# Optimization experiments

Measured on AMD Instinct MI355X. Metric: run time of the kernel, lower is better.

The kernel has to match this reference:

```python
import jax, jax.numpy as jnp
import numpy as np

B, C, H, W, MODES, RANK = 16, 128, 128, 128, 16, 8


def setup_inputs() -> dict:
    key = jax.random.key(0)
    ks = jax.random.split(key, 8)
    scale = 1.0 / (C * C)
    lr_scale = 0.02
    return {
        "x": jax.random.normal(ks[0], (B, C, H, W), dtype=jnp.float32),
        "w_real": scale * jax.random.normal(ks[1], (C, C, MODES, MODES), dtype=jnp.float32),
        "w_imag": scale * jax.random.normal(ks[2], (C, C, MODES, MODES), dtype=jnp.float32),
        "u_real": lr_scale * jax.random.normal(ks[3], (C, RANK, MODES, MODES), dtype=jnp.float32),
        "u_imag": lr_scale * jax.random.normal(ks[4], (C, RANK, MODES, MODES), dtype=jnp.float32),
        "v_real": lr_scale * jax.random.normal(ks[5], (C, RANK, MODES, MODES), dtype=jnp.float32),
        "v_imag": lr_scale * jax.random.normal(ks[6], (C, RANK, MODES, MODES), dtype=jnp.float32),
        "skip_w": (1.0 / np.sqrt(C)) * jax.random.normal(ks[7], (C, C), dtype=jnp.float32),
    }


def physical_act(x):
    # f(x) = x * exp(-|x|^2)
    return x * jnp.exp(-jnp.abs(x) ** 2)


def reference(x, w_real, w_imag, u_real, u_imag, v_real, v_imag, skip_w):
    Bb, Cc, Hh, Ww = x.shape
    # 1x1 conv skip path == channel matmul
    x_skip = jnp.einsum('oc,bchw->bohw', skip_w, x)
    # FFT to spectral domain: (B, C, H, W//2+1) complex64
    x_ft = jnp.fft.rfft2(x, norm='ortho')
    W_ft = x_ft.shape[-1]
    m1 = min(w_real.shape[-2], Hh)
    m2 = min(w_real.shape[-1], W_ft)
    # truncated-mode complex diagonal operator D (per-frequency channel mix)
    D = (w_real + 1j * w_imag)[:, :, :m1, :m2]          # (O, I, m1, m2)
    x_top = x_ft[:, :, :m1, :m2]                         # (B, I, m1, m2)
    out_top = jnp.einsum('bimn,oimn->bomn', x_top, D)
    # low-rank cross-frequency mixer UV*
    U = (u_real + 1j * u_imag)[:, :, :m1, :m2]           # (O, R, m1, m2)
    V = (v_real + 1j * v_imag)[:, :, :m1, :m2]           # (I, R, m1, m2)
    z = jnp.einsum('bimn,irmn->br', x_top, jnp.conj(V))  # (B, R)
    out_top = out_top + jnp.einsum('ormn,br->bomn', U, z)
    # scatter back into zero-padded full spectrum
    out_ft = jnp.zeros(x_ft.shape, dtype=x_ft.dtype).at[:, :, :m1, :m2].set(out_top)
    x_spectral = jnp.fft.irfft2(out_ft, s=(Hh, Ww), norm='ortho')
    out = x_spectral + x_skip
    return physical_act(out)
```

## Files before the change

kernel.cpp:

```cpp
#include <hip/hip_runtime.h>
#include <math.h>

#define TAB_OFF 0
#define XTOP_OFF 16384
#define Z_OFF (16384 + 1048576)
#define OTOP_OFF (Z_OFF + 256)
#define TF_OFF (OTOP_OFF + 1048576)
#define T2F_OFF (TF_OFF + 4096)
#define SWF_OFF XTOP_OFF

using bf16x8 = __attribute__((ext_vector_type(8))) short;
using s16x4  = __attribute__((ext_vector_type(4))) short;
using f32x16 = __attribute__((ext_vector_type(16))) float;

__device__ inline unsigned short bf_rnd(float v) {
  return (unsigned short)((__float_as_uint(v) + 0x8000u) >> 16);
}
__device__ inline void bf_split(float v, unsigned short& hi, unsigned short& lo) {
  unsigned u = __float_as_uint(v);
  hi = (unsigned short)(u >> 16);
  float r = v - __uint_as_float(u & 0xFFFF0000u);
  lo = (unsigned short)(__float_as_uint(r) >> 16);
}
__device__ inline bf16x8 ldfrag(const unsigned short* p) {
  s16x4 a = *(const s16x4*)p;
  s16x4 b = *(const s16x4*)(p + 4);
  bf16x8 r;
  r[0] = a[0]; r[1] = a[1]; r[2] = a[2]; r[3] = a[3];
  r[4] = b[0]; r[5] = b[1]; r[6] = b[2]; r[7] = b[3];
  return r;
}
__device__ inline bf16x8 ldfrag_sw(const unsigned short* base, int row, int koff) {
  int byte = row * 256 + ((koff * 2) ^ ((row & 7) << 4));
  return ldfrag((const unsigned short*)((const char*)base + byte));
}

__global__ __launch_bounds__(256) void k_tab(float* __restrict__ tab) {
  int idx = blockIdx.x * 256 + threadIdx.x;
  if (idx >= 16384) return;
  int which = idx >> 11, rem = idx & 2047;
  int a, j;
  if (which == 4 || which == 5) { a = rem & 127; j = rem >> 7; }
  else { a = rem >> 4; j = rem & 15; }
  int p = (a * j) & 127;
  float ang = (float)p * (float)(3.14159265358979323846 / 64.0);
  float cv = cosf(ang), sv = sinf(ang);
  float v;
  switch (which) {
    case 0: v = cv * (1.f / 128.f); break;
    case 1: v = -sv * (1.f / 128.f); break;
    case 2: v = cv; break;
    case 3: v = sv; break;
    case 4: v = cv; break;
    case 5: v = sv; break;
    case 6: v = ((rem & 15) == 0 ? 1.f : 2.f) * cv * (1.f / 128.f); break;
    default: v = ((rem & 15) == 0 ? 1.f : 2.f) * (-sv) * (1.f / 128.f); break;
  }
  tab[idx] = v;
}

__global__ __launch_bounds__(256) void k_fprep(unsigned short* __restrict__ tf) {
  int idx = blockIdx.x * 256 + threadIdx.x;
  if (idx >= 4096) return;
  int np = idx >> 7, k = idx & 127;
  int n = np & 15;
  int p = (k * n) & 127;
  float ang = (float)p * (float)(3.14159265358979323846 / 64.0);
  float v = (np < 16 ? cosf(ang) : -sinf(ang)) * (1.f / 128.f);
  unsigned short hi, lo;
  bf_split(v, hi, lo);
  tf[np * 128 + k] = hi;
  tf[4096 + np * 128 + k] = lo;
}

__global__ __launch_bounds__(256) void k_t2prep(const float* __restrict__ tab,
                                                unsigned short* __restrict__ t2f) {
  int idx = blockIdx.x * 256 + threadIdx.x;
  if (idx >= 4096) return;
  int w = idx >> 5, np = idx & 31;
  float v = (np < 16) ? tab[12288 + w * 16 + np] : tab[14336 + w * 16 + (np - 16)];
  t2f[idx] = bf_rnd(v);
}

__global__ __launch_bounds__(256) void k_wprep(const float* __restrict__ sw,
                                               unsigned short* __restrict__ swf) {
  int idx = blockIdx.x * 256 + threadIdx.x;
  if (idx >= 16384) return;
  int o = idx >> 7, k = idx & 127;
  unsigned short hb, lb;
  bf_split(sw[o * 128 + k], hb, lb);
  int kc = k >> 5, ks = (k >> 4) & 1, kh = (k >> 3) & 1, j = k & 7;
  int f0 = (kc * 2 + ks) * 2;
  swf[(f0 + 0) * 2048 + o * 16 + kh * 8 + j] = hb;
  swf[(f0 + 1) * 2048 + o * 16 + kh * 8 + j] = lb;
}

__global__ __launch_bounds__(256) void k_fwd(const float* __restrict__ x,
                                             const unsigned short* __restrict__ tf,
                                             const float* __restrict__ tab,
                                             float* __restrict__ xtop) {
  __shared__ unsigned short Xh[128 * 128];
  __shared__ unsigned short Tfh[32 * 128];
  __shared__ unsigned short Tfl[32 * 128];
  const int c = blockIdx.x, b = blockIdx.y;
  const int t = threadIdx.x;
  const int lane = t & 63, wv = t >> 6;

  #pragma unroll
  for (int it = 0; it < 32; ++it) {
    int idx = it * 256 + t;
    int part = idx >> 12, rem = idx & 4095;
    int row = rem >> 7, k = rem & 127;
    unsigned short v = tf[part * 4096 + rem];
    unsigned short* dst = part ? Tfl : Tfh;
    *(unsigned short*)((char*)dst + row * 256 + ((k * 2) ^ ((row & 7) << 4))) = v;
  }
  const float* img = x + (((size_t)(b * 128 + c)) << 14);
  #pragma unroll
  for (int it = 0; it < 16; ++it) {
    int flat = it * 256 + t;
    int h = flat >> 5, wq = flat & 31;
    float4 v = *(const float4*)(img + (size_t)flat * 4);
    s16x4 pk;
    pk[0] = (short)bf_rnd(v.x); pk[1] = (short)bf_rnd(v.y);
    pk[2] = (short)bf_rnd(v.z); pk[3] = (short)bf_rnd(v.w);
    *(s16x4*)((char*)Xh + h * 256 + ((wq * 8) ^ ((h & 7) << 4))) = pk;
  }
  __syncthreads();

  f32x16 acc;
  #pragma unroll
  for (int e = 0; e < 16; ++e) acc[e] = 0.f;
  const int orow = wv * 32 + (lane & 31);
  const int bcol = lane & 31;
  const int kh8 = (lane >> 5) * 8;
  #pragma unroll
  for (int kc8 = 0; kc8 < 8; ++kc8) {
    int kfull = kc8 * 16 + kh8;
    bf16x8 a  = ldfrag_sw(Xh, orow, kfull);
    bf16x8 th = ldfrag_sw(Tfh, bcol, kfull);
    bf16x8 tl = ldfrag_sw(Tfl, bcol, kfull);
    acc = __builtin_amdgcn_mfma_f32_32x32x16_bf16(a, th, acc, 0, 0, 0);
    acc = __builtin_amdgcn_mfma_f32_32x32x16_bf16(a, tl, acc, 0, 0, 0);
  }
  __syncthreads();

  float* Arp = (float*)Xh;
  float* Aip = Arp + 16 * 132;
  {
    const int col = lane & 31;
    #pragma unroll
    for (int r = 0; r < 16; ++r) {
      int h = wv * 32 + (r & 3) + 8 * (r >> 2) + 4 * (lane >> 5);
      if (col < 16) Arp[col * 132 + h] = acc[r];
      else          Aip[(col - 16) * 132 + h] = acc[r];
    }
  }
  __syncthreads();

  {
    const int m = t >> 4, n = t & 15;
    const float* tc = tab + 8192 + m * 128;
    const float* ts = tab + 10240 + m * 128;
    const float* ar = Arp + n * 132;
    const float* ai = Aip + n * 132;
    float xr = 0.f, xi = 0.f;
    #pragma unroll 8
    for (int h4 = 0; h4 < 128; h4 += 4) {
      float4 av = *(const float4*)(ar + h4);
      float4 iv = *(const float4*)(ai + h4);
      float4 cv = *(const float4*)(tc + h4);
      float4 sv = *(const float4*)(ts + h4);
      xr += av.x * cv.x + iv.x * sv.x;  xi += iv.x * cv.x - av.x * sv.x;
      xr += av.y * cv.y + iv.y * sv.y;  xi += iv.y * cv.y - av.y * sv.y;
      xr += av.z * cv.z + iv.z * sv.z;  xi += iv.z * cv.z - av.z * sv.z;
      xr += av.w * cv.w + iv.w * sv.w;  xi += iv.w * cv.w - av.w * sv.w;
    }
    size_t base = ((size_t)(b * 128 + c)) * 512 + (size_t)(m * 16 + n) * 2;
    xtop[base] = xr; xtop[base + 1] = xi;
  }
}

__global__ __launch_bounds__(256) void k_z(const float* __restrict__ xtop,
                                           const float* __restrict__ vre,
                                           const float* __restrict__ vim,
                                           float* __restrict__ zout) {
  int b = blockIdx.x, ic = blockIdx.y, t = threadIdx.x;
  float zr[8], zi[8];
  #pragma unroll
  for (int r = 0; r < 8; ++r) { zr[r] = 0.f; zi[r] = 0.f; }
  const float* xb = xtop + ((size_t)b * 128) * 512;
  for (int i = ic * 16; i < ic * 16 + 16; ++i) {
    float xr = xb[i * 512 + t * 2], xi = xb[i * 512 + t * 2 + 1];
    #pragma unroll
    for (int r = 0; r < 8; ++r) {
      float vr = vre[(size_t)(i * 8 + r) * 256 + t];
      float vi = vim[(size_t)(i * 8 + r) * 256 + t];
      zr[r] += xr * vr + xi * vi;
      zi[r] += xi * vr - xr * vi;
    }
  }
  #pragma unroll
  for (int r = 0; r < 8; ++r)
    for (int off = 32; off > 0; off >>= 1) {
      zr[r] += __shfl_down(zr[r], off);
      zi[r] += __shfl_down(zi[r], off);
    }
  __shared__ float red[4][16];
  int wid = t >> 6, lane = t & 63;
  if (lane == 0) {
    #pragma unroll
    for (int r = 0; r < 8; ++r) { red[wid][r * 2] = zr[r]; red[wid][r * 2 + 1] = zi[r]; }
  }
  __syncthreads();
  if (t < 16) atomicAdd(&zout[b * 16 + t], red[0][t] + red[1][t] + red[2][t] + red[3][t]);
}

__global__ __launch_bounds__(256) void k_mix(const float* __restrict__ xtop,
                                             const float* __restrict__ wre,
                                             const float* __restrict__ wim,
                                             const float* __restrict__ ure,
                                             const float* __restrict__ uim,
                                             const float* __restrict__ z,
                                             float* __restrict__ otop) {
  int o0 = blockIdx.x * 4, b0 = blockIdx.y * 2, ic = blockIdx.z, t = threadIdx.x;
  float ar[2][4], ai[2][4];
  #pragma unroll
  for (int bb = 0; bb < 2; ++bb)
    #pragma unroll
    for (int oo = 0; oo < 4; ++oo) { ar[bb][oo] = 0.f; ai[bb][oo] = 0.f; }
  const float* x0 = xtop + ((size_t)(b0 * 128)) * 512;
  const float* x1 = x0 + 128 * 512;
  for (int i = ic * 16; i < ic * 16 + 16; ++i) {
    float x0r = x0[i * 512 + t * 2], x0i = x0[i * 512 + t * 2 + 1];
    float x1r = x1[i * 512 + t * 2], x1i = x1[i * 512 + t * 2 + 1];
    #pragma unroll
    for (int oo = 0; oo < 4; ++oo) {
      size_t di = (size_t)((o0 + oo) * 128 + i) * 256 + t;
      float dr = wre[di], dj = wim[di];
      ar[0][oo] += dr * x0r - dj * x0i; ai[0][oo] += dr * x0i + dj * x0r;
      ar[1][oo] += dr * x1r - dj * x1i; ai[1][oo] += dr * x1i + dj * x1r;
    }
  }
  if (ic == 0) {
    float zr[2][8], zi[2][8];
    #pragma unroll
    for (int bb = 0; bb < 2; ++bb)
      #pragma unroll
      for (int r = 0; r < 8; ++r) {
        zr[bb][r] = z[(b0 + bb) * 16 + r * 2];
        zi[bb][r] = z[(b0 + bb) * 16 + r * 2 + 1];
      }
    #pragma unroll
    for (int oo = 0; oo < 4; ++oo)
      #pragma unroll
      for (int r = 0; r < 8; ++r) {
        float urv = ure[(size_t)((o0 + oo) * 8 + r) * 256 + t];
        float uiv = uim[(size_t)((o0 + oo) * 8 + r) * 256 + t];
        #pragma unroll
        for (int bb = 0; bb < 2; ++bb) {
          ar[bb][oo] += urv * zr[bb][r] - uiv * zi[bb][r];
          ai[bb][oo] += urv * zi[bb][r] + uiv * zr[bb][r];
        }
      }
  }
  #pragma unroll
  for (int bb = 0; bb < 2; ++bb)
    #pragma unroll
    for (int oo = 0; oo < 4; ++oo) {
      size_t oi = ((size_t)((b0 + bb) * 128 + o0 + oo) * 256 + (size_t)t) * 2;
      atomicAdd(&otop[oi], ar[bb][oo]);
      atomicAdd(&otop[oi + 1], ai[bb][oo]);
    }
}

__global__ __launch_bounds__(256) void k_out(const float* __restrict__ x,
                                             const unsigned short* __restrict__ swf,
                                             const unsigned short* __restrict__ t2f,
                                             const float* __restrict__ otop,
                                             const float* __restrict__ tab,
                                             float* __restrict__ out) {
  __shared__ unsigned short Ylds[128 * 36];
  __shared__ unsigned short Bh[128 * 36], Bl[128 * 36];
  const int h = blockIdx.x, b = blockIdx.y;
  const int t = threadIdx.x;
  const int lane = t & 63, wv = t >> 6;
  const int kh8 = (lane >> 5) * 8;
  const int col = lane & 31;
  const int o_lane = wv * 32 + col;

  const int cofs = t >> 7;
  const int wB = t & 127;
  const float* xbase = x + (size_t)b * 2097152 + (size_t)h * 128 + wB;
  float xv[16], xn[16];
  #pragma unroll
  for (int it = 0; it < 16; ++it)
    xv[it] = xbase[(size_t)(it * 2 + cofs) * 16384];

  {
    int o = t >> 1, nh = (t & 1) * 8;
    float yr[8], yi[8];
    #pragma unroll
    for (int j = 0; j < 8; ++j) { yr[j] = 0.f; yi[j] = 0.f; }
    const float* xb = otop + ((size_t)(b * 128 + o)) * 512 + nh * 2;
    #pragma unroll 4
    for (int m = 0; m < 16; ++m) {
      float cm = tab[4096 + h * 16 + m];
      float sm = tab[6144 + h * 16 + m];
      float4 q0 = *(const float4*)(xb + m * 32 + 0);
      float4 q1 = *(const float4*)(xb + m * 32 + 4);
      float4 q2 = *(const float4*)(xb + m * 32 + 8);
      float4 q3 = *(const float4*)(xb + m * 32 + 12);
      yr[0] += q0.x * cm - q0.y * sm; yi[0] += q0.x * sm + q0.y * cm;
      yr[1] += q0.z * cm - q0.w * sm; yi[1] += q0.z * sm + q0.w * cm;
      yr[2] += q1.x * cm - q1.y * sm; yi[2] += q1.x * sm + q1.y * cm;
      yr[3] += q1.z * cm - q1.w * sm; yi[3] += q1.z * sm + q1.w * cm;
      yr[4] += q2.x * cm - q2.y * sm; yi[4] += q2.x * sm + q2.y * cm;
      yr[5] += q2.z * cm - q2.w * sm; yi[5] += q2.z * sm + q2.w * cm;
      yr[6] += q3.x * cm - q3.y * sm; yi[6] += q3.x * sm + q3.y * cm;
      yr[7] += q3.z * cm - q3.w * sm; yi[7] += q3.z * sm + q3.w * cm;
    }
    #pragma unroll
    for (int j = 0; j < 8; ++j) {
      Ylds[o * 36 + nh + j] = bf_rnd(yr[j]);
      Ylds[o * 36 + 16 + nh + j] = bf_rnd(yi[j]);
    }
  }
  __syncthreads();

  f32x16 acc[4];
  #pragma unroll
  for (int nt = 0; nt < 4; ++nt)
    #pragma unroll
    for (int e = 0; e < 16; ++e) acc[nt][e] = 0.f;

  #pragma unroll
  for (int kc = 0; kc < 4; ++kc) {
    {
      #pragma unroll
      for (int it = 0; it < 16; ++it) {
        int cl = it * 2 + cofs;
        unsigned short hb, lb;
        bf_split(xv[it], hb, lb);
        Bh[wB * 36 + cl] = hb; Bl[wB * 36 + cl] = lb;
      }
    }
    bf16x8 ah[2], al[2];
    #pragma unroll
    for (int ks = 0; ks < 2; ++ks) {
      const unsigned short* base = swf + (size_t)((kc * 2 + ks) * 2) * 2048 + o_lane * 16 + kh8;
      ah[ks] = *(const bf16x8*)base;
      al[ks] = *(const bf16x8*)(base + 2048);
    }
    if (kc < 3) {
      #pragma unroll
      for (int it = 0; it < 16; ++it)
        xn[it] = xbase[(size_t)((kc + 1) * 32 + it * 2 + cofs) * 16384];
    }
    __syncthreads();
    #pragma unroll
    for (int ks = 0; ks < 2; ++ks) {
      const int kb = ks * 16 + kh8;
      #pragma unroll
      for (int nt = 0; nt < 4; ++nt) {
        bf16x8 bh_ = ldfrag(&Bh[(nt * 32 + col) * 36 + kb]);
        bf16x8 bl_ = ldfrag(&Bl[(nt * 32 + col) * 36 + kb]);
        acc[nt] = __builtin_amdgcn_mfma_f32_32x32x16_bf16(ah[ks], bh_, acc[nt], 0, 0, 0);
        acc[nt] = __builtin_amdgcn_mfma_f32_32x32x16_bf16(ah[ks], bl_, acc[nt], 0, 0, 0);
        acc[nt] = __builtin_amdgcn_mfma_f32_32x32x16_bf16(al[ks], bh_, acc[nt], 0, 0, 0);
      }
    }
    __syncthreads();
    if (kc < 3) {
      #pragma unroll
      for (int it = 0; it < 16; ++it) xv[it] = xn[it];
    }
  }

  #pragma unroll
  for (int ks = 0; ks < 2; ++ks) {
    const int kb = ks * 16 + kh8;
    bf16x8 ya = ldfrag(&Ylds[o_lane * 36 + kb]);
    #pragma unroll
    for (int nt = 0; nt < 4; ++nt) {
      bf16x8 tb = *(const bf16x8*)(t2f + (nt * 32 + col) * 32 + kb);
      acc[nt] = __builtin_amdgcn_mfma_f32_32x32x16_bf16(ya, tb, acc[nt], 0, 0, 0);
    }
  }

  #pragma unroll
  for (int nt = 0; nt < 4; ++nt) {
    int w = nt * 32 + col;
    #pragma unroll
    for (int r = 0; r < 16; ++r) {
      int o = wv * 32 + (r & 3) + 8 * (r >> 2) + 4 * (lane >> 5);
      float v = acc[nt][r];
      out[((size_t)(b * 128 + o)) * 16384 + (size_t)h * 128 + w] = v * __expf(-v * v);
    }
  }
}

extern "C" void kernel_launch(void* const* d_in, const int* in_sizes, int n_in,
                              void* d_out, int out_size, void* d_ws, size_t ws_size,
                              hipStream_t stream) {
  const float* x  = (const float*)d_in[0];
  const float* wr = (const float*)d_in[1];
  const float* wi = (const float*)d_in[2];
  const float* ur = (const float*)d_in[3];
  const float* ui = (const float*)d_in[4];
  const float* vr = (const float*)d_in[5];
  const float* vi = (const float*)d_in[6];
  const float* sw = (const float*)d_in[7];
  float* out  = (float*)d_out;
  float* ws   = (float*)d_ws;
  float* tab  = ws + TAB_OFF;
  float* xtop = ws + XTOP_OFF;
  float* z    = ws + Z_OFF;
  float* otop = ws + OTOP_OFF;
  unsigned short* tf  = (unsigned short*)(ws + TF_OFF);
  unsigned short* t2f = (unsigned short*)(ws + T2F_OFF);
  unsigned short* swf = (unsigned short*)(ws + SWF_OFF);

  hipMemsetAsync(z, 0, 256 * sizeof(float), stream);
  hipMemsetAsync(otop, 0, 1048576 * sizeof(float), stream);
  hipLaunchKernelGGL(k_tab, dim3(64), dim3(256), 0, stream, tab);
  hipLaunchKernelGGL(k_fprep, dim3(16), dim3(256), 0, stream, tf);
  hipLaunchKernelGGL(k_t2prep, dim3(16), dim3(256), 0, stream, tab, t2f);
  hipLaunchKernelGGL(k_fwd, dim3(128, 16), dim3(256), 0, stream, x, tf, tab, xtop);
  hipLaunchKernelGGL(k_z,   dim3(16, 8), dim3(256), 0, stream, xtop, vr, vi, z);
  hipLaunchKernelGGL(k_mix, dim3(32, 8, 8), dim3(256), 0, stream, xtop, wr, wi, ur, ui, z, otop);
  hipLaunchKernelGGL(k_wprep, dim3(64), dim3(256), 0, stream, sw, swf);
  hipLaunchKernelGGL(k_out, dim3(128, 16), dim3(256), 0, stream, x, swf, t2f, otop, tab, out);
}
```

Before: 204.3 us.

## Merge prep kernels into one launch and fuse z reduction into forward FFT

Four small table and weight prep kernels are combined into a single k_prep launch, with t2f now computed directly instead of read back from tab, and swf moved to its own workspace region. The low-rank z projection is computed inside k_fwd from the per-block spectral values still in registers, using warp shuffles and one atomic per block, which removes the separate k_z kernel and its reread of xtop. This cuts launch count and global traffic, in exchange for more atomics on z (2048 blocks contending for 256 addresses) and a little extra work at the end of k_fwd.

Result: faster. 195.6 us (-4.3%).

```diff
diff --git a/kernel.cpp b/kernel.cpp
--- a/kernel.cpp
+++ b/kernel.cpp
@@ -7,7 +7,7 @@
 #define OTOP_OFF (Z_OFF + 256)
 #define TF_OFF (OTOP_OFF + 1048576)
 #define T2F_OFF (TF_OFF + 4096)
-#define SWF_OFF XTOP_OFF
+#define SWF_OFF (T2F_OFF + 2048)
 
 using bf16x8 = __attribute__((ext_vector_type(8))) short;
 using s16x4  = __attribute__((ext_vector_type(4))) short;
@@ -35,73 +35,75 @@
   return ldfrag((const unsigned short*)((const char*)base + byte));
 }
 
-__global__ __launch_bounds__(256) void k_tab(float* __restrict__ tab) {
+__global__ __launch_bounds__(256) void k_prep(const float* __restrict__ sw,
+                                              float* __restrict__ tab,
+                                              unsigned short* __restrict__ tf,
+                                              unsigned short* __restrict__ t2f,
+                                              unsigned short* __restrict__ swf) {
   int idx = blockIdx.x * 256 + threadIdx.x;
-  if (idx >= 16384) return;
-  int which = idx >> 11, rem = idx & 2047;
-  int a, j;
-  if (which == 4 || which == 5) { a = rem & 127; j = rem >> 7; }
-  else { a = rem >> 4; j = rem & 15; }
-  int p = (a * j) & 127;
-  float ang = (float)p * (float)(3.14159265358979323846 / 64.0);
-  float cv = cosf(ang), sv = sinf(ang);
-  float v;
-  switch (which) {
-    case 0: v = cv * (1.f / 128.f); break;
-    case 1: v = -sv * (1.f / 128.f); break;
-    case 2: v = cv; break;
-    case 3: v = sv; break;
-    case 4: v = cv; break;
-    case 5: v = sv; break;
-    case 6: v = ((rem & 15) == 0 ? 1.f : 2.f) * cv * (1.f / 128.f); break;
-    default: v = ((rem & 15) == 0 ? 1.f : 2.f) * (-sv) * (1.f / 128.f); break;
-  }
-  tab[idx] = v;
-}
-
-__global__ __launch_bounds__(256) void k_fprep(unsigned short* __restrict__ tf) {
-  int idx = blockIdx.x * 256 + threadIdx.x;
-  if (idx >= 4096) return;
-  int np = idx >> 7, k = idx & 127;
-  int n = np & 15;
-  int p = (k * n) & 127;
-  float ang = (float)p * (float)(3.14159265358979323846 / 64.0);
-  float v = (np < 16 ? cosf(ang) : -sinf(ang)) * (1.f / 128.f);
-  unsigned short hi, lo;
-  bf_split(v, hi, lo);
-  tf[np * 128 + k] = hi;
-  tf[4096 + np * 128 + k] = lo;
-}
-
-__global__ __launch_bounds__(256) void k_t2prep(const float* __restrict__ tab,
-                                                unsigned short* __restrict__ t2f) {
-  int idx = blockIdx.x * 256 + threadIdx.x;
-  if (idx >= 4096) return;
-  int w = idx >> 5, np = idx & 31;
-  float v = (np < 16) ? tab[12288 + w * 16 + np] : tab[14336 + w * 16 + (np - 16)];
-  t2f[idx] = bf_rnd(v);
-}
-
-__global__ __launch_bounds__(256) void k_wprep(const float* __restrict__ sw,
-                                               unsigned short* __restrict__ swf) {
-  int idx = blockIdx.x * 256 + threadIdx.x;
-  if (idx >= 16384) return;
-  int o = idx >> 7, k = idx & 127;
-  unsigned short hb, lb;
-  bf_split(sw[o * 128 + k], hb, lb);
-  int kc = k >> 5, ks = (k >> 4) & 1, kh = (k >> 3) & 1, j = k & 7;
-  int f0 = (kc * 2 + ks) * 2;
-  swf[(f0 + 0) * 2048 + o * 16 + kh * 8 + j] = hb;
-  swf[(f0 + 1) * 2048 + o * 16 + kh * 8 + j] = lb;
+  if (idx < 16384) {
+    int which = idx >> 11, rem = idx & 2047;
+    int a, j;
+    if (which == 4 || which == 5) { a = rem & 127; j = rem >> 7; }
+    else { a = rem >> 4; j = rem & 15; }
+    int p = (a * j) & 127;
+    float ang = (float)p * (float)(3.14159265358979323846 / 64.0);
+    float cv = cosf(ang), sv = sinf(ang);
+    float v;
+    switch (which) {
+      case 0: v = cv * (1.f / 128.f); break;
+      case 1: v = -sv * (1.f / 128.f); break;
+      case 2: v = cv; break;
+      case 3: v = sv; break;
+      case 4: v = cv; break;
+      case 5: v = sv; break;
+      case 6: v = ((rem & 15) == 0 ? 1.f : 2.f) * cv * (1.f / 128.f); break;
+      default: v = ((rem & 15) == 0 ? 1.f : 2.f) * (-sv) * (1.f / 128.f); break;
+    }
+    tab[idx] = v;
+  } else if (idx < 20480) {
+    int r = idx - 16384;
+    int np = r >> 7, k = r & 127;
+    int n = np & 15;
+    int p = (k * n) & 127;
+    float ang = (float)p * (float)(3.14159265358979323846 / 64.0);
+    float v = (np < 16 ? cosf(ang) : -sinf(ang)) * (1.f / 128.f);
+    unsigned short hi, lo;
+    bf_split(v, hi, lo);
+    tf[np * 128 + k] = hi;
+    tf[4096 + np * 128 + k] = lo;
+  } else if (idx < 24576) {
+    int r = idx - 20480;
+    int w = r >> 5, np = r & 31;
+    int n = np & 15;
+    int p = (w * n) & 127;
+    float ang = (float)p * (float)(3.14159265358979323846 / 64.0);
+    float cn = (n == 0) ? 1.f : 2.f;
+    float v = (np < 16 ? cosf(ang) : -sinf(ang)) * cn * (1.f / 128.f);
+    t2f[r] = bf_rnd(v);
+  } else {
+    int r = idx - 24576;
+    int o = r >> 7, k = r & 127;
+    unsigned short hb, lb;
+    bf_split(sw[o * 128 + k], hb, lb);
+    int kc = k >> 5, ks = (k >> 4) & 1, kh = (k >> 3) & 1, j = k & 7;
+    int f0 = (kc * 2 + ks) * 2;
+    swf[(f0 + 0) * 2048 + o * 16 + kh * 8 + j] = hb;
+    swf[(f0 + 1) * 2048 + o * 16 + kh * 8 + j] = lb;
+  }
 }
 
 __global__ __launch_bounds__(256) void k_fwd(const float* __restrict__ x,
                                              const unsigned short* __restrict__ tf,
                                              const float* __restrict__ tab,
-                                             float* __restrict__ xtop) {
+                                             const float* __restrict__ vre,
+                                             const float* __restrict__ vim,
+                                             float* __restrict__ xtop,
+                                             float* __restrict__ zout) {
   __shared__ unsigned short Xh[128 * 128];
   __shared__ unsigned short Tfh[32 * 128];
   __shared__ unsigned short Tfl[32 * 128];
+  __shared__ float red[4][16];
   const int c = blockIdx.x, b = blockIdx.y;
   const int t = threadIdx.x;
   const int lane = t & 63, wv = t >> 6;
@@ -158,13 +160,13 @@
   }
   __syncthreads();
 
+  float xr = 0.f, xi = 0.f;
   {
     const int m = t >> 4, n = t & 15;
     const float* tc = tab + 8192 + m * 128;
     const float* ts = tab + 10240 + m * 128;
     const float* ar = Arp + n * 132;
     const float* ai = Aip + n * 132;
-    float xr = 0.f, xi = 0.f;
     #pragma unroll 8
     for (int h4 = 0; h4 < 128; h4 += 4) {
       float4 av = *(const float4*)(ar + h4);
@@ -176,44 +178,32 @@
       xr += av.z * cv.z + iv.z * sv.z;  xi += iv.z * cv.z - av.z * sv.z;
       xr += av.w * cv.w + iv.w * sv.w;  xi += iv.w * cv.w - av.w * sv.w;
     }
-    size_t base = ((size_t)(b * 128 + c)) * 512 + (size_t)(m * 16 + n) * 2;
+    size_t base = ((size_t)(b * 128 + c)) * 512 + (size_t)t * 2;
     xtop[base] = xr; xtop[base + 1] = xi;
   }
-}
-
-__global__ __launch_bounds__(256) void k_z(const float* __restrict__ xtop,
-                                           const float* __restrict__ vre,
-                                           const float* __restrict__ vim,
-                                           float* __restrict__ zout) {
-  int b = blockIdx.x, ic = blockIdx.y, t = threadIdx.x;
-  float zr[8], zi[8];
-  #pragma unroll
-  for (int r = 0; r < 8; ++r) { zr[r] = 0.f; zi[r] = 0.f; }
-  const float* xb = xtop + ((size_t)b * 128) * 512;
-  for (int i = ic * 16; i < ic * 16 + 16; ++i) {
-    float xr = xb[i * 512 + t * 2], xi = xb[i * 512 + t * 2 + 1];
+
+  {
+    float zr[8], zi[8];
     #pragma unroll
     for (int r = 0; r < 8; ++r) {
-      float vr = vre[(size_t)(i * 8 + r) * 256 + t];
-      float vi = vim[(size_t)(i * 8 + r) * 256 + t];
-      zr[r] += xr * vr + xi * vi;
-      zi[r] += xi * vr - xr * vi;
-    }
-  }
-  #pragma unroll
-  for (int r = 0; r < 8; ++r)
-    for (int off = 32; off > 0; off >>= 1) {
-      zr[r] += __shfl_down(zr[r], off);
-      zi[r] += __shfl_down(zi[r], off);
-    }
-  __shared__ float red[4][16];
-  int wid = t >> 6, lane = t & 63;
-  if (lane == 0) {
-    #pragma unroll
-    for (int r = 0; r < 8; ++r) { red[wid][r * 2] = zr[r]; red[wid][r * 2 + 1] = zi[r]; }
-  }
-  __syncthreads();
-  if (t < 16) atomicAdd(&zout[b * 16 + t], red[0][t] + red[1][t] + red[2][t] + red[3][t]);
+      float vr = vre[(size_t)(c * 8 + r) * 256 + t];
+      float vi = vim[(size_t)(c * 8 + r) * 256 + t];
+      zr[r] = xr * vr + xi * vi;
+      zi[r] = xi * vr - xr * vi;
+    }
+    #pragma unroll
+    for (int r = 0; r < 8; ++r)
+      for (int off = 32; off > 0; off >>= 1) {
+        zr[r] += __shfl_down(zr[r], off);
+        zi[r] += __shfl_down(zi[r], off);
+      }
+    if (lane == 0) {
+      #pragma unroll
+      for (int r = 0; r < 8; ++r) { red[wv][r * 2] = zr[r]; red[wv][r * 2 + 1] = zi[r]; }
+    }
+    __syncthreads();
+    if (t < 16) atomicAdd(&zout[b * 16 + t], red[0][t] + red[1][t] + red[2][t] + red[3][t]);
+  }
 }
 
 __global__ __launch_bounds__(256) void k_mix(const float* __restrict__ xtop,
@@ -423,12 +413,8 @@
 
   hipMemsetAsync(z, 0, 256 * sizeof(float), stream);
   hipMemsetAsync(otop, 0, 1048576 * sizeof(float), stream);
-  hipLaunchKernelGGL(k_tab, dim3(64), dim3(256), 0, stream, tab);
-  hipLaunchKernelGGL(k_fprep, dim3(16), dim3(256), 0, stream, tf);
-  hipLaunchKernelGGL(k_t2prep, dim3(16), dim3(256), 0, stream, tab, t2f);
-  hipLaunchKernelGGL(k_fwd, dim3(128, 16), dim3(256), 0, stream, x, tf, tab, xtop);
-  hipLaunchKernelGGL(k_z,   dim3(16, 8), dim3(256), 0, stream, xtop, vr, vi, z);
-  hipLaunchKernelGGL(k_mix, dim3(32, 8, 8), dim3(256), 0, stream, xtop, wr, wi, ur, ui, z, otop);
-  hipLaunchKernelGGL(k_wprep, dim3(64), dim3(256), 0, stream, sw, swf);
-  hipLaunchKernelGGL(k_out, dim3(128, 16), dim3(256), 0, stream, x, swf, t2f, otop, tab, out);
-}
+  hipLaunchKernelGGL(k_prep, dim3(160), dim3(256), 0, stream, sw, tab, tf, t2f, swf);
+  hipLaunchKernelGGL(k_fwd,  dim3(128, 16), dim3(256), 0, stream, x, tf, tab, vr, vi, xtop, z);
+  hipLaunchKernelGGL(k_mix,  dim3(32, 8, 8), dim3(256), 0, stream, xtop, wr, wi, ur, ui, z, otop);
+  hipLaunchKernelGGL(k_out,  dim3(128, 16), dim3(256), 0, stream, x, swf, t2f, otop, tab, out);
+}
```
